# Optimization experiments

Measured on AMD Instinct MI355X. Metric: run time of the kernel, lower is better.

Reference implementation:

```python
import jax, jax.numpy as jnp
import numpy as np

F_, H_, W_ = 6, 16, 28          # latent video grid (frames, height, width)
DIM, NH = 1536, 12
HD = DIM // NH                   # 128
L = F_ * H_ * W_                 # 2688 tokens
EPS = 1e-6
BLOCK = 3 * H_ * W_              # block_causal_size = 3*frame_height*frame_width


def setup_inputs() -> dict:
    key = jax.random.key(0)
    ks = jax.random.split(key, 8)
    def lin(k):
        return jax.random.normal(k, (DIM, DIM), jnp.float32) * 0.02
    x = jax.random.normal(ks[0], (1, L, DIM), jnp.float32)
    # RoPE freqs: unit-modulus complex numbers stored as [...,(re,im)]
    ang = jax.random.uniform(ks[1], (1024, HD // 2), jnp.float32, -np.pi, np.pi)
    freqs = jnp.stack([jnp.cos(ang), jnp.sin(ang)], axis=-1)  # [1024, 64, 2]
    return {
        'x': x,
        'seq_lens': jnp.array([L], jnp.int32),
        'grid_sizes': jnp.array([[F_, H_, W_]], jnp.int32),
        'freqs': freqs,
        'Wq': lin(ks[2]), 'bq': jnp.zeros((DIM,), jnp.float32),
        'Wk': lin(ks[3]), 'bk': jnp.zeros((DIM,), jnp.float32),
        'Wv': lin(ks[4]), 'bv': jnp.zeros((DIM,), jnp.float32),
        'Wo': lin(ks[5]), 'bo': jnp.zeros((DIM,), jnp.float32),
        'gq': jnp.ones((DIM,), jnp.float32),
        'gk': jnp.ones((DIM,), jnp.float32),
    }


def _rmsnorm(x, g):
    # WanRMSNorm: x * rsqrt(mean(x^2) + eps) * weight
    return x * jax.lax.rsqrt(jnp.mean(x * x, axis=-1, keepdims=True) + EPS) * g


def _rope_apply(x, F, H, W, freqs, start_frame=0):
    # x: [B, L, n, d]; freqs: [1024, d//2, 2] (re, im). Per-axis split [c0, c3, c3].
    B, Lx, n, d = x.shape
    c = d // 2
    c3 = c // 3
    c0 = c - 2 * c3
    f0 = freqs[start_frame:start_frame + F, :c0]      # [F, c0, 2]
    f1 = freqs[:H, c0:c0 + c3]                        # [H, c3, 2]
    f2 = freqs[:W, c0 + c3:]                          # [W, c3, 2]
    ff = jnp.concatenate([
        jnp.broadcast_to(f0[:, None, None], (F, H, W, c0, 2)),
        jnp.broadcast_to(f1[None, :, None], (F, H, W, c3, 2)),
        jnp.broadcast_to(f2[None, None, :], (F, H, W, c3, 2)),
    ], axis=3).reshape(Lx, 1, c, 2)                   # [L, 1, c, 2]
    xr = x.reshape(B, Lx, n, c, 2)
    xre, xim = xr[..., 0], xr[..., 1]
    fre, fim = ff[None, ..., 0], ff[None, ..., 1]     # broadcast over batch, heads
    ore = xre * fre - xim * fim
    oim = xre * fim + xim * fre
    return jnp.stack([ore, oim], axis=-1).reshape(B, Lx, n, d)


def reference(x, seq_lens, grid_sizes, freqs, Wq, bq, Wk, bk, Wv, bv, Wo, bo, gq, gk):
    b, s = x.shape[:2]
    F = int(grid_sizes[0, 0]); H = int(grid_sizes[0, 1]); W = int(grid_sizes[0, 2])
    q = _rmsnorm(x @ Wq + bq, gq).reshape(b, s, NH, HD)
    k = _rmsnorm(x @ Wk + bk, gk).reshape(b, s, NH, HD)
    v = (x @ Wv + bv).reshape(b, s, NH, HD)
    rq = _rope_apply(q, F, H, W, freqs)
    rk = _rope_apply(k, F, H, W, freqs)
    # block-causal attention: query attends to keys in same-or-earlier 3-frame block
    scores = jnp.einsum('bihd,bjhd->bhij', rq, rk) * (HD ** -0.5)
    blk = jnp.arange(s) // (3 * H * W)
    mask = blk[None, :] <= blk[:, None]               # [s, s]
    scores = jnp.where(mask[None, None], scores, -1e30)
    attn = jax.nn.softmax(scores, axis=-1)
    out = jnp.einsum('bhij,bjhd->bihd', attn, v).reshape(b, s, DIM)
    return out @ Wo + bo
```

## Files before the change

kernel.cpp:

```cpp
#include <hip/hip_runtime.h>

#define L_SEQ 2688
#define DIM   1536
#define NH    12
#define HD    128
#define BLK_TOK 1344
#define HW_   448
#define W_    28

typedef unsigned short u16;
typedef unsigned int   u32;
typedef __attribute__((ext_vector_type(4))) float f32x4;
typedef __attribute__((ext_vector_type(16))) float f32x16;
typedef __attribute__((ext_vector_type(8))) short s16x8;
typedef __attribute__((ext_vector_type(2))) int i32x2;
typedef __attribute__((ext_vector_type(4))) u32 u32x4;

__device__ __forceinline__ u16 f2b(float f) {
    u32 u = __builtin_bit_cast(u32, f);
    return (u16)((u + 0x7FFFu + ((u >> 16) & 1u)) >> 16);
}
__device__ __forceinline__ float b2f(u16 b) {
    return __builtin_bit_cast(float, (u32)b << 16);
}
__device__ __forceinline__ u32 cvt_pk_bf16(float lo, float hi) {
    u32 r;
    asm("v_cvt_pk_bf16_f32 %0, %1, %2" : "=v"(r) : "v"(lo), "v"(hi));
    return r;
}

__global__ __launch_bounds__(256) void k_cvt_x(const float* __restrict__ x,
                                               u16* __restrict__ xb, int n4) {
    int i = blockIdx.x * 256 + threadIdx.x;
    int stride = gridDim.x * 256;
    for (; i < n4; i += stride) {
        float4 v = ((const float4*)x)[i];
        ushort4 o;
        o.x = f2b(v.x); o.y = f2b(v.y); o.z = f2b(v.z); o.w = f2b(v.w);
        ((ushort4*)xb)[i] = o;
    }
}

__global__ __launch_bounds__(256) void k_trans_w(const float* __restrict__ w0,
                                                 const float* __restrict__ w1,
                                                 const float* __restrict__ w2,
                                                 const float* __restrict__ w3,
                                                 u16* __restrict__ wt_all) {
    const float* w = blockIdx.z == 0 ? w0 : blockIdx.z == 1 ? w1 : blockIdx.z == 2 ? w2 : w3;
    u16* wt = wt_all + (size_t)blockIdx.z * DIM * DIM;
    __shared__ float t[64][65];
    const int k0 = blockIdx.y * 64, n0 = blockIdx.x * 64;
    const int c = threadIdx.x & 63, rg = threadIdx.x >> 6;
#pragma unroll
    for (int it = 0; it < 16; ++it) {
        int r = rg * 16 + it;
        t[r][c] = w[(size_t)(k0 + r) * DIM + n0 + c];
    }
    __syncthreads();
#pragma unroll
    for (int it = 0; it < 16; ++it) {
        int r = rg * 16 + it;
        wt[(size_t)(n0 + r) * DIM + k0 + c] = f2b(t[c][r]);
    }
}

template<int OUTF>
__global__ __launch_bounds__(256, 2) void k_gemm(const u16* __restrict__ A,
                                                 const u16* __restrict__ Bt_all,
                                                 const float* __restrict__ b0,
                                                 const float* __restrict__ b1,
                                                 const float* __restrict__ b2,
                                                 void* __restrict__ out_all) {
    const int z = blockIdx.z;
    const u16* Bt = Bt_all + (size_t)z * DIM * DIM;
    const float* bias = z == 0 ? b0 : z == 1 ? b1 : b2;

    __shared__ u16 lA[128 * 32];
    __shared__ u16 lB[128 * 32];
    const int tid = threadIdx.x, lane = tid & 63, wid = tid >> 6;
    const int wm = wid >> 1, wn = wid & 1;
    const int bm = blockIdx.y, bn = blockIdx.x;
    const int lr = lane & 15, lg = lane >> 4;

    f32x4 acc[4][4] = {};

    for (int kt = 0; kt < DIM / 32; ++kt) {
#pragma unroll
        for (int i = 0; i < 2; ++i) {
            int s = wid * 128 + i * 64 + lane;
            int row = s >> 2, c16 = s & 3;
            const u16* ga = A + (size_t)(bm * 128 + row) * DIM + kt * 32 + c16 * 8;
            __builtin_amdgcn_global_load_lds(
                (const __attribute__((address_space(1))) u32*)ga,
                (__attribute__((address_space(3))) u32*)&lA[(wid * 128 + i * 64) * 8],
                16, 0, 0);
            const u16* gb = Bt + (size_t)(bn * 128 + row) * DIM + kt * 32 + c16 * 8;
            __builtin_amdgcn_global_load_lds(
                (const __attribute__((address_space(1))) u32*)gb,
                (__attribute__((address_space(3))) u32*)&lB[(wid * 128 + i * 64) * 8],
                16, 0, 0);
        }
        __syncthreads();
        s16x8 af[4], bf[4];
#pragma unroll
        for (int m = 0; m < 4; ++m)
            af[m] = *(const s16x8*)&lA[(wm * 64 + m * 16 + lr) * 32 + lg * 8];
#pragma unroll
        for (int n = 0; n < 4; ++n)
            bf[n] = *(const s16x8*)&lB[(wn * 64 + n * 16 + lr) * 32 + lg * 8];
#pragma unroll
        for (int m = 0; m < 4; ++m)
#pragma unroll
            for (int n = 0; n < 4; ++n)
                acc[m][n] = __builtin_amdgcn_mfma_f32_16x16x32_bf16(af[m], bf[n], acc[m][n], 0, 0, 0);
        __syncthreads();
    }
#pragma unroll
    for (int n = 0; n < 4; ++n) {
        int col = bn * 128 + wn * 64 + n * 16 + lr;
        float bv = bias[col];
#pragma unroll
        for (int m = 0; m < 4; ++m) {
            int row0 = bm * 128 + wm * 64 + m * 16 + lg * 4;
#pragma unroll
            for (int r = 0; r < 4; ++r) {
                float v = acc[m][n][r] + bv;
                if (OUTF)
                    ((float*)out_all)[(size_t)(row0 + r) * DIM + col] = v;
                else
                    ((u16*)out_all)[(size_t)z * L_SEQ * DIM + (size_t)(row0 + r) * DIM + col] = f2b(v);
            }
        }
    }
}

__global__ __launch_bounds__(256) void k_norm_rope(const u16* __restrict__ pre_all,
                                                   const float* __restrict__ gq,
                                                   const float* __restrict__ gk,
                                                   const float* __restrict__ freqs,
                                                   u16* __restrict__ qh,
                                                   u16* __restrict__ kh) {
    const int which = blockIdx.y;
    const u16* pre = pre_all + (size_t)which * L_SEQ * DIM;
    const float* g = which ? gk : gq;
    u16* outh = which ? kh : qh;

    const int i = blockIdx.x;
    const int t = threadIdx.x;
    const u32* prow = (const u32*)(pre + (size_t)i * DIM);

    float re[3], im[3];
    float ss = 0.f;
#pragma unroll
    for (int a = 0; a < 3; ++a) {
        u32 p = prow[t + a * 256];
        float x = b2f((u16)(p & 0xFFFFu)), y = b2f((u16)(p >> 16));
        re[a] = x; im[a] = y;
        ss += x * x + y * y;
    }
#pragma unroll
    for (int o = 32; o > 0; o >>= 1) ss += __shfl_down(ss, o, 64);
    __shared__ float sred[4];
    if ((t & 63) == 0) sred[t >> 6] = ss;
    __syncthreads();
    float rms = rsqrtf((sred[0] + sred[1] + sred[2] + sred[3]) * (1.0f / DIM) + 1e-6f);

    const int f = i / HW_;
    const int rem = i - f * HW_;
    const int hp = rem / W_;
    const int wp = rem - hp * W_;
#pragma unroll
    for (int a = 0; a < 3; ++a) {
        int j = t + a * 256;
        int h = j >> 6, pj = j & 63;
        float2 gg = ((const float2*)g)[j];
        float x = re[a] * rms * gg.x;
        float y = im[a] * rms * gg.y;
        int ridx = pj < 22 ? f : (pj < 43 ? hp : wp);
        float2 cs = ((const float2*)freqs)[ridx * 64 + pj];
        float ore = x * cs.x - y * cs.y;
        float oim = x * cs.y + y * cs.x;
        u32 o = (u32)f2b(ore) | ((u32)f2b(oim) << 16);
        ((u32*)outh)[(size_t)h * (L_SEQ * 64) + (size_t)i * 64 + pj] = o;
    }
}

__global__ __launch_bounds__(256) void k_vtrans(const u16* __restrict__ vpre,
                                                u16* __restrict__ vt) {
    const int i0 = blockIdx.x * 64, d0 = blockIdx.y * 64, h = blockIdx.z;
    __shared__ u16 t[64][68];
    const int c = threadIdx.x & 63, rg = threadIdx.x >> 6;
#pragma unroll
    for (int it = 0; it < 16; ++it) {
        int r = rg * 16 + it;
        t[r][c] = vpre[(size_t)(i0 + r) * DIM + h * HD + d0 + c];
    }
    __syncthreads();
#pragma unroll
    for (int it = 0; it < 16; ++it) {
        int r = rg * 16 + it;
        vt[(size_t)h * (HD * L_SEQ) + (size_t)(d0 + r) * L_SEQ + i0 + c] = t[c][r];
    }
}

__global__ __launch_bounds__(256, 2) void k_attn(const u16* __restrict__ qh,
                                                 const u16* __restrict__ kh,
                                                 const u16* __restrict__ vt,
                                                 u16* __restrict__ ob,
                                                 float* __restrict__ Opart,
                                                 float* __restrict__ mlp) {
    __shared__ char lsm[2][32768];

    const int flat = blockIdx.x;
    const int xcd = flat & 7, idx = flat >> 3;
    const int work = (xcd < 4) ? (xcd * 95 + idx) : (380 + (xcd - 4) * 94 + idx);
    const int head = work / 63;
    const int bx = work - head * 63;
    int qt, kv0, mode;
    if (bx < 21)      { qt = bx;      kv0 = 0;  mode = 0; }
    else if (bx < 42) { qt = bx;      kv0 = 0;  mode = 1; }
    else              { qt = bx - 21; kv0 = 21; mode = 2; }

    const int tid = threadIdx.x, lane = tid & 63, w = tid >> 6;
    const int pairI = w >> 1;
    const int qhalf = w & 1;
    const int q31 = lane & 31, hi = lane >> 5;
    const size_t hOff = (size_t)head * ((size_t)L_SEQ * HD);
    const u16* Kh = kh + hOff;
    const u16* Vh = vt + hOff;
    const int qrow0 = qt * 64 + qhalf * 32;

    s16x8 aq[8];
#pragma unroll
    for (int kk = 0; kk < 8; ++kk)
        aq[kk] = *(const s16x8*)&qh[hOff + (size_t)(qrow0 + q31) * HD + kk * 16 + hi * 8];

    const int pt = tid & 127;
    const int rh = pt >> 4, ck = pt & 15;
    const int rv = pt >> 3, cvv = pt & 7;
    char* slot = lsm[pairI];

#define STAGE_TILE(TG)                                                            \
    {                                                                             \
        _Pragma("unroll")                                                         \
        for (int i = 0; i < 8; ++i) {                                             \
            const u16* src = Kh + (size_t)((TG) * 64 + i * 8 + rh) * HD + 8 * (ck ^ ((i & 1) * 8 + rh)); \
            __builtin_amdgcn_global_load_lds(                                     \
                (const __attribute__((address_space(1))) u32*)src,                \
                (__attribute__((address_space(3))) u32*)(slot + i * 2048 + pt * 16), 16, 0, 0); \
        }                                                                         \
        _Pragma("unroll")                                                         \
        for (int i = 0; i < 8; ++i) {                                             \
            const u16* src = Vh + (size_t)(i * 16 + rv) * L_SEQ + (TG) * 64 + 8 * (cvv ^ (rv & 7)); \
            __builtin_amdgcn_global_load_lds(                                     \
                (const __attribute__((address_space(1))) u32*)src,                \
                (__attribute__((address_space(3))) u32*)(slot + 16384 + i * 2048 + pt * 16), 16, 0, 0); \
        }                                                                         \
    }

    f32x16 acc[4] = {};
    float mrun = -1e30f, lrun = 0.f;
    const float sc2 = 0.12751739646917983f;

    if (pairI == 0) STAGE_TILE(kv0);
    __syncthreads();
    for (int ph = 1; ph <= 21; ++ph) {
        const int pst = ph & 1;
        if (pairI == pst && ph <= 20) STAGE_TILE(kv0 + ph);
        if (pairI == (pst ^ 1)) {
            f32x16 sv[2] = {};
            __builtin_amdgcn_s_setprio(1);
#pragma unroll
            for (int js = 0; js < 2; ++js)
#pragma unroll
                for (int kk = 0; kk < 8; ++kk) {
                    int off = (js * 32 + q31) * 256 + ((kk * 32 + hi * 16) ^ ((q31 & 15) << 4));
                    s16x8 kf = *(const s16x8*)(slot + off);
                    sv[js] = __builtin_amdgcn_mfma_f32_32x32x16_bf16(kf, aq[kk], sv[js], 0, 0, 0);
                }
            __builtin_amdgcn_s_setprio(0);

            float mx = fmaxf(sv[0][0], sv[1][0]);
#pragma unroll
            for (int e = 1; e < 16; ++e) mx = fmaxf(mx, fmaxf(sv[0][e], sv[1][e]));
            mx = fmaxf(mx, __shfl_xor(mx, 32, 64));
            mx *= sc2;
            const int resc = (mx - mrun) > 11.5f;
            const float mm = resc ? mx : mrun;
            const float fac = resc ? __builtin_amdgcn_exp2f(mrun - mm) : 1.0f;
            mrun = mm;
            float sum = 0.f;
#pragma unroll
            for (int js = 0; js < 2; ++js)
#pragma unroll
                for (int e = 0; e < 16; ++e) {
                    float pv = __builtin_amdgcn_exp2f(sv[js][e] * sc2 - mm);
                    sv[js][e] = pv;
                    sum += pv;
                }
            sum += __shfl_xor(sum, 32, 64);
            lrun = lrun * fac + sum;
            if (__any(resc)) {
#pragma unroll
                for (int ds = 0; ds < 4; ++ds)
#pragma unroll
                    for (int e = 0; e < 16; ++e) acc[ds][e] *= fac;
            }

            s16x8 pa[4];
#pragma unroll
            for (int js = 0; js < 2; ++js)
#pragma unroll
                for (int hf = 0; hf < 2; ++hf) {
                    u32 a0 = cvt_pk_bf16(sv[js][hf * 8 + 0], sv[js][hf * 8 + 1]);
                    u32 a1 = cvt_pk_bf16(sv[js][hf * 8 + 2], sv[js][hf * 8 + 3]);
                    u32 b0 = cvt_pk_bf16(sv[js][hf * 8 + 4], sv[js][hf * 8 + 5]);
                    u32 b1 = cvt_pk_bf16(sv[js][hf * 8 + 6], sv[js][hf * 8 + 7]);
                    i32x2 r0 = __builtin_amdgcn_permlane32_swap((int)a0, (int)b0, false, false);
                    i32x2 r1 = __builtin_amdgcn_permlane32_swap((int)a1, (int)b1, false, false);
                    u32x4 fw;
                    fw.x = (u32)r0.x; fw.y = (u32)r1.x; fw.z = (u32)r0.y; fw.w = (u32)r1.y;
                    pa[js * 2 + hf] = __builtin_bit_cast(s16x8, fw);
                }

            __builtin_amdgcn_s_setprio(1);
#pragma unroll
            for (int jstep = 0; jstep < 4; ++jstep)
#pragma unroll
                for (int ds = 0; ds < 4; ++ds) {
                    int off = 16384 + (ds * 32 + q31) * 128 + ((jstep * 32 + hi * 16) ^ ((q31 & 7) << 4));
                    s16x8 vf = *(const s16x8*)(slot + off);
                    acc[ds] = __builtin_amdgcn_mfma_f32_32x32x16_bf16(vf, pa[jstep], acc[ds], 0, 0, 0);
                }
            __builtin_amdgcn_s_setprio(0);
        }
        __syncthreads();
    }

    float2* mlb = (float2*)(lsm[1]);
    char* accb = lsm[0];
    if (w >= 2) {
        char* base = accb + qhalf * 16384 + lane * 256;
#pragma unroll
        for (int ds = 0; ds < 4; ++ds)
#pragma unroll
            for (int g = 0; g < 4; ++g) {
                f32x4 v4;
#pragma unroll
                for (int e = 0; e < 4; ++e) v4[e] = acc[ds][g * 4 + e];
                *(f32x4*)(base + (((ds * 4 + g) * 16) ^ ((lane & 15) << 4))) = v4;
            }
        if (hi == 0) {
            float2 t2; t2.x = mrun; t2.y = lrun;
            mlb[qhalf * 32 + q31] = t2;
        }
    }
    __syncthreads();
    if (w < 2) {
        float2 ml2 = mlb[qhalf * 32 + q31];
        float M = fmaxf(mrun, ml2.x);
        float wa = exp2f(mrun - M), wb = exp2f(ml2.x - M);
        lrun = lrun * wa + ml2.y * wb;
        mrun = M;
        const char* base = accb + qhalf * 16384 + lane * 256;
#pragma unroll
        for (int ds = 0; ds < 4; ++ds)
#pragma unroll
            for (int g = 0; g < 4; ++g) {
                f32x4 v4 = *(const f32x4*)(base + (((ds * 4 + g) * 16) ^ ((lane & 15) << 4)));
#pragma unroll
                for (int e = 0; e < 4; ++e) acc[ds][g * 4 + e] = acc[ds][g * 4 + e] * wa + v4[e] * wb;
            }
        if (mode == 0) {
            const float inv = 1.0f / lrun;
            u16* orow = ob + (size_t)(qrow0 + q31) * DIM + head * HD;
#pragma unroll
            for (int ds = 0; ds < 4; ++ds)
#pragma unroll
                for (int g = 0; g < 4; ++g) {
                    uint2 pk2;
                    pk2.x = cvt_pk_bf16(acc[ds][g * 4 + 0] * inv, acc[ds][g * 4 + 1] * inv);
                    pk2.y = cvt_pk_bf16(acc[ds][g * 4 + 2] * inv, acc[ds][g * 4 + 3] * inv);
                    *(uint2*)(orow + ds * 32 + g * 8 + hi * 4) = pk2;
                }
        } else {
            const int pairo = (head * 21 + (qt - 21)) * 2 + (mode - 1);
            float* Op = Opart + (size_t)pairo * (64 * 128);
            const int rowl = qhalf * 32 + q31;
#pragma unroll
            for (int ds = 0; ds < 4; ++ds)
#pragma unroll
                for (int g = 0; g < 4; ++g) {
                    float4 v4;
                    v4.x = acc[ds][g * 4 + 0]; v4.y = acc[ds][g * 4 + 1];
                    v4.z = acc[ds][g * 4 + 2]; v4.w = acc[ds][g * 4 + 3];
                    *(float4*)(&Op[rowl * 128 + ds * 32 + g * 8 + hi * 4]) = v4;
                }
            if (hi == 0) {
                float2 t2; t2.x = mrun; t2.y = lrun;
                ((float2*)mlp)[(size_t)pairo * 64 + rowl] = t2;
            }
        }
    }
#undef STAGE_TILE
}

__global__ __launch_bounds__(256) void k_merge(const float* __restrict__ Opart,
                                               const float* __restrict__ mlp,
                                               u16* __restrict__ ob) {
    const int b = blockIdx.x;
    const int qt2 = b % 21, head = b / 21;
    const int pair = head * 21 + qt2;
    const float* O0 = Opart + (size_t)pair * 2 * 8192;
    const float* O1 = O0 + 8192;
    const int tid = threadIdx.x;
    const int row = tid >> 2, cs = (tid & 3) * 32;
    float2 a = ((const float2*)mlp)[(size_t)pair * 2 * 64 + row];
    float2 c = ((const float2*)mlp)[(size_t)(pair * 2 + 1) * 64 + row];
    float M = fmaxf(a.x, c.x);
    float w0 = exp2f(a.x - M), w1 = exp2f(c.x - M);
    float inv = 1.0f / (w0 * a.y + w1 * c.y);
    w0 *= inv; w1 *= inv;
    const int rowg = BLK_TOK + qt2 * 64 + row;
    u32* orow = (u32*)(ob + (size_t)rowg * DIM + head * HD + cs);
    const float4* p0 = (const float4*)(O0 + row * 128 + cs);
    const float4* p1 = (const float4*)(O1 + row * 128 + cs);
#pragma unroll
    for (int u = 0; u < 8; ++u) {
        float4 x0 = p0[u], x1 = p1[u];
        float o0 = x0.x * w0 + x1.x * w1;
        float o1 = x0.y * w0 + x1.y * w1;
        float o2 = x0.z * w0 + x1.z * w1;
        float o3 = x0.w * w0 + x1.w * w1;
        orow[u * 2]     = (u32)f2b(o0) | ((u32)f2b(o1) << 16);
        orow[u * 2 + 1] = (u32)f2b(o2) | ((u32)f2b(o3) << 16);
    }
}

extern "C" void kernel_launch(void* const* d_in, const int* in_sizes, int n_in,
                              void* d_out, int out_size, void* d_ws, size_t ws_size,
                              hipStream_t stream) {
    const float* x     = (const float*)d_in[0];
    const float* freqs = (const float*)d_in[3];
    const float* Wq    = (const float*)d_in[4];
    const float* bq    = (const float*)d_in[5];
    const float* Wk    = (const float*)d_in[6];
    const float* bk    = (const float*)d_in[7];
    const float* Wv    = (const float*)d_in[8];
    const float* bv    = (const float*)d_in[9];
    const float* Wo    = (const float*)d_in[10];
    const float* bo    = (const float*)d_in[11];
    const float* gq    = (const float*)d_in[12];
    const float* gk    = (const float*)d_in[13];

    const size_t LD = (size_t)L_SEQ * DIM;
    u16* wt_all  = (u16*)d_ws;
    u16* xb      = wt_all + (size_t)4 * DIM * DIM;
    u16* pre_all = xb + LD;
    u16* qh      = pre_all + 3 * LD;
    u16* kh2     = qh + LD;
    u16* vt      = kh2 + LD;
    u16* ob      = vt + LD;
    float* Opart = (float*)pre_all;
    float* mlp   = Opart + (size_t)12 * 21 * 2 * 64 * 128;

    k_cvt_x<<<2016, 256, 0, stream>>>(x, xb, (int)(LD / 4));
    k_trans_w<<<dim3(24, 24, 4), 256, 0, stream>>>(Wq, Wk, Wv, Wo, wt_all);
    k_gemm<0><<<dim3(12, 21, 3), 256, 0, stream>>>(xb, wt_all, bq, bk, bv, pre_all);
    k_norm_rope<<<dim3(L_SEQ, 2), 256, 0, stream>>>(pre_all, gq, gk, freqs, qh, kh2);
    k_vtrans<<<dim3(42, 2, NH), 256, 0, stream>>>(pre_all + 2 * LD, vt);
    k_attn<<<dim3(756), 256, 0, stream>>>(qh, kh2, vt, ob, Opart, mlp);
    k_merge<<<dim3(252), 256, 0, stream>>>(Opart, mlp, ob);
    k_gemm<1><<<dim3(12, 21, 1), 256, 0, stream>>>(ob, wt_all + (size_t)3 * DIM * DIM, bo, bo, bo, d_out);
}
```

Before: 184.5 us.

## Split each KV tile across both wave pairs instead of ping-pong producer/consumer

Previously the two wave pairs alternated, with one pair staging the next K/V tile while the other computed on the current tile. Now all four waves stage each tile together into a double buffer and each pair computes on half of the tile's keys (32 of 64). This keeps every wave doing MFMA work each iteration. The per-pair partial softmax states then get combined by the existing merge epilogue. It changes the swizzle pattern for K staging and relies on the merge logic treating the pairs as independent key partitions.

```diff
diff --git a/kernel.cpp b/kernel.cpp
--- a/kernel.cpp
+++ b/kernel.cpp
@@ -235,105 +235,101 @@
     for (int kk = 0; kk < 8; ++kk)
         aq[kk] = *(const s16x8*)&qh[hOff + (size_t)(qrow0 + q31) * HD + kk * 16 + hi * 8];
 
-    const int pt = tid & 127;
-    const int rh = pt >> 4, ck = pt & 15;
-    const int rv = pt >> 3, cvv = pt & 7;
-    char* slot = lsm[pairI];
-
-#define STAGE_TILE(TG)                                                            \
+    const int rh = tid >> 4, ck = tid & 15;
+    const int rv = tid >> 3, cv = tid & 7;
+    const int koff = 8 * (ck ^ rh);
+    const int voff = 8 * (cv ^ (rv & 7));
+
+#define STAGE_TILE(TG, BUF)                                                       \
     {                                                                             \
+        char* dst = lsm[BUF];                                                     \
         _Pragma("unroll")                                                         \
-        for (int i = 0; i < 8; ++i) {                                             \
-            const u16* src = Kh + (size_t)((TG) * 64 + i * 8 + rh) * HD + 8 * (ck ^ ((i & 1) * 8 + rh)); \
+        for (int i = 0; i < 4; ++i) {                                             \
+            const u16* src = Kh + (size_t)((TG) * 64 + i * 16 + rh) * HD + koff;  \
             __builtin_amdgcn_global_load_lds(                                     \
                 (const __attribute__((address_space(1))) u32*)src,                \
-                (__attribute__((address_space(3))) u32*)(slot + i * 2048 + pt * 16), 16, 0, 0); \
+                (__attribute__((address_space(3))) u32*)(dst + i * 4096 + tid * 16), 16, 0, 0); \
         }                                                                         \
         _Pragma("unroll")                                                         \
-        for (int i = 0; i < 8; ++i) {                                             \
-            const u16* src = Vh + (size_t)(i * 16 + rv) * L_SEQ + (TG) * 64 + 8 * (cvv ^ (rv & 7)); \
+        for (int i = 0; i < 4; ++i) {                                             \
+            const u16* src = Vh + (size_t)(i * 32 + rv) * L_SEQ + (TG) * 64 + voff; \
             __builtin_amdgcn_global_load_lds(                                     \
                 (const __attribute__((address_space(1))) u32*)src,                \
-                (__attribute__((address_space(3))) u32*)(slot + 16384 + i * 2048 + pt * 16), 16, 0, 0); \
+                (__attribute__((address_space(3))) u32*)(dst + 16384 + i * 4096 + tid * 16), 16, 0, 0); \
         }                                                                         \
     }
 
     f32x16 acc[4] = {};
     float mrun = -1e30f, lrun = 0.f;
     const float sc2 = 0.12751739646917983f;
-
-    if (pairI == 0) STAGE_TILE(kv0);
+    const int krow = pairI * 32 + q31;
+
+    STAGE_TILE(kv0, 0);
     __syncthreads();
-    for (int ph = 1; ph <= 21; ++ph) {
-        const int pst = ph & 1;
-        if (pairI == pst && ph <= 20) STAGE_TILE(kv0 + ph);
-        if (pairI == (pst ^ 1)) {
-            f32x16 sv[2] = {};
-            __builtin_amdgcn_s_setprio(1);
-#pragma unroll
-            for (int js = 0; js < 2; ++js)
-#pragma unroll
-                for (int kk = 0; kk < 8; ++kk) {
-                    int off = (js * 32 + q31) * 256 + ((kk * 32 + hi * 16) ^ ((q31 & 15) << 4));
-                    s16x8 kf = *(const s16x8*)(slot + off);
-                    sv[js] = __builtin_amdgcn_mfma_f32_32x32x16_bf16(kf, aq[kk], sv[js], 0, 0, 0);
-                }
-            __builtin_amdgcn_s_setprio(0);
-
-            float mx = fmaxf(sv[0][0], sv[1][0]);
-#pragma unroll
-            for (int e = 1; e < 16; ++e) mx = fmaxf(mx, fmaxf(sv[0][e], sv[1][e]));
-            mx = fmaxf(mx, __shfl_xor(mx, 32, 64));
-            mx *= sc2;
-            const int resc = (mx - mrun) > 11.5f;
-            const float mm = resc ? mx : mrun;
-            const float fac = resc ? __builtin_amdgcn_exp2f(mrun - mm) : 1.0f;
-            mrun = mm;
-            float sum = 0.f;
-#pragma unroll
-            for (int js = 0; js < 2; ++js)
-#pragma unroll
-                for (int e = 0; e < 16; ++e) {
-                    float pv = __builtin_amdgcn_exp2f(sv[js][e] * sc2 - mm);
-                    sv[js][e] = pv;
-                    sum += pv;
-                }
-            sum += __shfl_xor(sum, 32, 64);
-            lrun = lrun * fac + sum;
-            if (__any(resc)) {
-#pragma unroll
-                for (int ds = 0; ds < 4; ++ds)
-#pragma unroll
-                    for (int e = 0; e < 16; ++e) acc[ds][e] *= fac;
+    for (int t = 0; t < 21; ++t) {
+        if (t < 20) STAGE_TILE(kv0 + t + 1, (t + 1) & 1);
+        const char* slot = lsm[t & 1];
+
+        f32x16 sv = {};
+        __builtin_amdgcn_s_setprio(1);
+#pragma unroll
+        for (int kk = 0; kk < 8; ++kk) {
+            int off = krow * 256 + ((kk * 32 + hi * 16) ^ ((q31 & 15) << 4));
+            s16x8 kf = *(const s16x8*)(slot + off);
+            sv = __builtin_amdgcn_mfma_f32_32x32x16_bf16(kf, aq[kk], sv, 0, 0, 0);
+        }
+        __builtin_amdgcn_s_setprio(0);
+
+        float mx = sv[0];
+#pragma unroll
+        for (int e = 1; e < 16; ++e) mx = fmaxf(mx, sv[e]);
+        mx = fmaxf(mx, __shfl_xor(mx, 32, 64));
+        mx *= sc2;
+        const int resc = (mx - mrun) > 11.5f;
+        const float mm = resc ? mx : mrun;
+        const float fac = resc ? __builtin_amdgcn_exp2f(mrun - mm) : 1.0f;
+        mrun = mm;
+        float sum = 0.f;
+#pragma unroll
+        for (int e = 0; e < 16; ++e) {
+            float pv = __builtin_amdgcn_exp2f(sv[e] * sc2 - mm);
+            sv[e] = pv;
+            sum += pv;
+        }
+        sum += __shfl_xor(sum, 32, 64);
+        lrun = lrun * fac + sum;
+        if (__any(resc)) {
+#pragma unroll
+            for (int ds = 0; ds < 4; ++ds)
+#pragma unroll
+                for (int e = 0; e < 16; ++e) acc[ds][e] *= fac;
+        }
+
+        s16x8 pa[2];
+#pragma unroll
+        for (int hf = 0; hf < 2; ++hf) {
+            u32 a0 = cvt_pk_bf16(sv[hf * 8 + 0], sv[hf * 8 + 1]);
+            u32 a1 = cvt_pk_bf16(sv[hf * 8 + 2], sv[hf * 8 + 3]);
+            u32 b0 = cvt_pk_bf16(sv[hf * 8 + 4], sv[hf * 8 + 5]);
+            u32 b1 = cvt_pk_bf16(sv[hf * 8 + 6], sv[hf * 8 + 7]);
+            i32x2 r0 = __builtin_amdgcn_permlane32_swap((int)a0, (int)b0, false, false);
+            i32x2 r1 = __builtin_amdgcn_permlane32_swap((int)a1, (int)b1, false, false);
+            u32x4 fw;
+            fw.x = (u32)r0.x; fw.y = (u32)r1.x; fw.z = (u32)r0.y; fw.w = (u32)r1.y;
+            pa[hf] = __builtin_bit_cast(s16x8, fw);
+        }
+
+        __builtin_amdgcn_s_setprio(1);
+#pragma unroll
+        for (int jstep = 0; jstep < 2; ++jstep)
+#pragma unroll
+            for (int ds = 0; ds < 4; ++ds) {
+                int off = 16384 + (ds * 32 + q31) * 128 +
+                          ((pairI * 64 + jstep * 32 + hi * 16) ^ ((q31 & 7) << 4));
+                s16x8 vf = *(const s16x8*)(slot + off);
+                acc[ds] = __builtin_amdgcn_mfma_f32_32x32x16_bf16(vf, pa[jstep], acc[ds], 0, 0, 0);
             }
-
-            s16x8 pa[4];
-#pragma unroll
-            for (int js = 0; js < 2; ++js)
-#pragma unroll
-                for (int hf = 0; hf < 2; ++hf) {
-                    u32 a0 = cvt_pk_bf16(sv[js][hf * 8 + 0], sv[js][hf * 8 + 1]);
-                    u32 a1 = cvt_pk_bf16(sv[js][hf * 8 + 2], sv[js][hf * 8 + 3]);
-                    u32 b0 = cvt_pk_bf16(sv[js][hf * 8 + 4], sv[js][hf * 8 + 5]);
-                    u32 b1 = cvt_pk_bf16(sv[js][hf * 8 + 6], sv[js][hf * 8 + 7]);
-                    i32x2 r0 = __builtin_amdgcn_permlane32_swap((int)a0, (int)b0, false, false);
-                    i32x2 r1 = __builtin_amdgcn_permlane32_swap((int)a1, (int)b1, false, false);
-                    u32x4 fw;
-                    fw.x = (u32)r0.x; fw.y = (u32)r1.x; fw.z = (u32)r0.y; fw.w = (u32)r1.y;
-                    pa[js * 2 + hf] = __builtin_bit_cast(s16x8, fw);
-                }
-
-            __builtin_amdgcn_s_setprio(1);
-#pragma unroll
-            for (int jstep = 0; jstep < 4; ++jstep)
-#pragma unroll
-                for (int ds = 0; ds < 4; ++ds) {
-                    int off = 16384 + (ds * 32 + q31) * 128 + ((jstep * 32 + hi * 16) ^ ((q31 & 7) << 4));
-                    s16x8 vf = *(const s16x8*)(slot + off);
-                    acc[ds] = __builtin_amdgcn_mfma_f32_32x32x16_bf16(vf, pa[jstep], acc[ds], 0, 0, 0);
-                }
-            __builtin_amdgcn_s_setprio(0);
-        }
+        __builtin_amdgcn_s_setprio(0);
         __syncthreads();
     }
 
```

New measurement: 171.9 us. 1.07x faster.
